# Optimization experiments

Measured on AMD Instinct MI355X. Metric: run time of the kernel, lower is better.

Reference implementation:

```python
import jax, jax.numpy as jnp
import numpy as np

HEADS = 12
LN_EPS = 1e-5


def setup_inputs() -> dict:
    B, S, D = 2, 2048, 768
    k = jax.random.key(0)
    ks = jax.random.split(k, 16)
    std = 0.02
    inp = {
        "key": jax.random.normal(ks[0], (B, S, D), jnp.float32),
        "query": jax.random.normal(ks[1], (B, S, D), jnp.float32),
        "value": jax.random.normal(ks[2], (B, S, D), jnp.float32),
        "mask": jax.random.randint(ks[3], (B, S, S), 0, 2).astype(bool),
        "Wk_w": jax.random.normal(ks[4], (D, D), jnp.float32) * std,
        "Wk_b": jnp.zeros((D,), jnp.float32),
        "Wq_w": jax.random.normal(ks[5], (D, D), jnp.float32) * std,
        "Wq_b": jnp.zeros((D,), jnp.float32),
        "Wv_w": jax.random.normal(ks[6], (D, D), jnp.float32) * std,
        "Wv_b": jnp.zeros((D,), jnp.float32),
        "Wc_w": jax.random.normal(ks[7], (D, D), jnp.float32) * std,
        "Wc_b": jnp.zeros((D,), jnp.float32),
        "ln_g": jnp.ones((D,), jnp.float32),
        "ln_b": jnp.zeros((D,), jnp.float32),
    }
    return inp


def _mha(key, query, value, mask, Wk_w, Wk_b, Wq_w, Wq_b, Wv_w, Wv_b,
         Wc_w, Wc_b, ln_g, ln_b):
    B, Sq, D = query.shape
    Sk = key.shape[1]
    H = HEADS
    hd = D // H
    scaler = np.float32(D ** 0.5)  # NOTE: source scales by sqrt(hidden_size), not sqrt(head_dim)

    # QKV projections (torch Linear: x @ W.T + b)
    hk = (key @ Wk_w.T + Wk_b).reshape(B, Sk, H, hd).transpose(2, 0, 1, 3)    # (H,B,Sk,hd)
    hq = (query @ Wq_w.T + Wq_b).reshape(B, Sq, H, hd).transpose(2, 0, 1, 3)  # (H,B,Sq,hd)
    hv = (value @ Wv_w.T + Wv_b).reshape(B, Sk, H, hd).transpose(2, 0, 1, 3)  # (H,B,Sk,hd)

    qk = jnp.einsum('hbqd,hbkd->hbqk', hq, hk) / scaler
    qk = jnp.where(mask[None], -jnp.inf, qk)  # mask repeated over heads in source
    attn = jax.nn.softmax(qk, axis=-1)        # dropout is identity in eval
    out = jnp.einsum('hbqk,hbkd->hbqd', attn, hv)  # (H,B,Sq,hd)

    # Faithful replication of source reshape chain:
    # (H*B,Sq,hd).view(B,H,Sq,hd).permute(1,2,0,3).view(B,Sq,D)
    out = out.reshape(B, H, Sq, hd)             # flat reinterpretation, head-major data
    out = jnp.transpose(out, (1, 2, 0, 3)).reshape(B, Sq, D)

    out = out @ Wc_w.T + Wc_b                   # Wconcat; dropout identity
    x = out + query                             # residual
    mu = jnp.mean(x, axis=-1, keepdims=True)
    var = jnp.mean((x - mu) ** 2, axis=-1, keepdims=True)
    return ln_g * (x - mu) / jnp.sqrt(var + LN_EPS) + ln_b


def reference(key, query, value, mask, Wk_w, Wk_b, Wq_w, Wq_b, Wv_w, Wv_b,
              Wc_w, Wc_b, ln_g, ln_b):
    return _mha(key, query, value, mask, Wk_w, Wk_b, Wq_w, Wq_b,
                Wv_w, Wv_b, Wc_w, Wc_b, ln_g, ln_b)
```

## Files before the change

### kernel.cpp

```cpp
#include <hip/hip_runtime.h>
#include <stdint.h>

typedef float v4f __attribute__((ext_vector_type(4)));
typedef short v8s __attribute__((ext_vector_type(8)));

#define AS1 __attribute__((address_space(1)))
#define AS3 __attribute__((address_space(3)))

__device__ __forceinline__ void load16_to_lds(const void* g, void* l) {
  __builtin_amdgcn_global_load_lds((AS1 void*)g, (AS3 void*)l, 16, 0, 0);
}
__device__ __forceinline__ void load4_to_lds(const void* g, void* l) {
  __builtin_amdgcn_global_load_lds((AS1 void*)g, (AS3 void*)l, 4, 0, 0);
}

__device__ __forceinline__ float fexp2(float x) {
#if __has_builtin(__builtin_amdgcn_exp2f)
  return __builtin_amdgcn_exp2f(x);
#else
  return exp2f(x);
#endif
}

__device__ __forceinline__ unsigned short f2bf_rn(float f) {
  union { float f; uint32_t u; } v; v.f = f;
  return (unsigned short)((v.u + 0x8000u) >> 16);
}
__device__ __forceinline__ uint32_t pack_bf2(float x, float y) {
  union { float f; uint32_t u; } a, b; a.f = x; b.f = y;
  return __builtin_amdgcn_perm(b.u + 0x8000u, a.u + 0x8000u, 0x07060302u);
}

#define QSCALE 0.052058786f

__global__ __launch_bounds__(256) void pack_mask_kernel(
    const uint32_t* __restrict__ mask, uint32_t* __restrict__ bits) {
  __shared__ int s_i32;
  const int tid = threadIdx.x;
  if (tid == 0) s_i32 = 1;
  __syncthreads();
  if (mask[tid] > 1u) s_i32 = 0;
  __syncthreads();
  if (s_i32) {
    const int lane = tid & 63;
    const int gw = (blockIdx.x * 256 + tid) >> 6;
#pragma unroll 4
    for (int it = 0; it < 32; ++it) {
      const size_t base = (size_t)gw * 2048 + it * 64;
      unsigned long long bal = __ballot(mask[base + lane] != 0u);
      if (lane == 0) *(unsigned long long*)&bits[base >> 5] = bal;
    }
  } else {
    const int wi = blockIdx.x * 256 + tid;
    const uint32_t* p = mask + (size_t)wi * 8;
    uint32_t w = 0;
#pragma unroll
    for (int j8 = 0; j8 < 8; ++j8) {
      uint32_t u = p[j8];
#pragma unroll
      for (int k = 0; k < 4; ++k)
        w |= (((u >> (8 * k)) & 0xFFu) ? 1u : 0u) << (j8 * 4 + k);
    }
    bits[wi] = w;
  }
}

__global__ __launch_bounds__(256) void conv_w_kernel(
    const float* __restrict__ wk, const float* __restrict__ wq,
    const float* __restrict__ wv, const float* __restrict__ wc,
    unsigned short* __restrict__ dk, unsigned short* __restrict__ dq,
    unsigned short* __restrict__ dv, unsigned short* __restrict__ dc) {
  const int y = blockIdx.y;
  const float* s; unsigned short* d; float sc = 1.f;
  if (y == 0)      { s = wk; d = dk; }
  else if (y == 1) { s = wq; d = dq; sc = QSCALE; }
  else if (y == 2) { s = wv; d = dv; }
  else             { s = wc; d = dc; }
  const int i = blockIdx.x * 256 + threadIdx.x;
  float4 f = ((const float4*)s)[i];
  uint2 o;
  o.x = pack_bf2(f.x * sc, f.y * sc);
  o.y = pack_bf2(f.z * sc, f.w * sc);
  ((uint2*)d)[i] = o;
}

__global__ __launch_bounds__(256) void gemm_qkv_kernel(
    const float* __restrict__ q_in, const float* __restrict__ k_in,
    const float* __restrict__ v_in,
    const unsigned short* __restrict__ wqb, const unsigned short* __restrict__ wkb,
    const unsigned short* __restrict__ wvb,
    const float* __restrict__ bq, const float* __restrict__ bk,
    const float* __restrict__ bv,
    unsigned short* __restrict__ Qb, unsigned short* __restrict__ Kb,
    unsigned short* __restrict__ Vt) {
  const int which = blockIdx.z;
  const float* A; const unsigned short* Wb; const float* bias; float bscale;
  if (which == 0)      { A = q_in; Wb = wqb; bias = bq; bscale = QSCALE; }
  else if (which == 1) { A = k_in; Wb = wkb; bias = bk; bscale = 1.f; }
  else                 { A = v_in; Wb = wvb; bias = bv; bscale = 1.f; }

  const int m0 = blockIdx.x * 128, n0 = blockIdx.y * 128;
  const int tid = threadIdx.x, lane = tid & 63, wid = tid >> 6;
  const int wm = wid >> 1, wn = wid & 1;
  const int l16 = lane & 15, quad = lane >> 4;

  __shared__ __align__(16) unsigned short As[128 * 32];
  __shared__ __align__(16) unsigned short Bs[128 * 32];

  v4f acc[4][4];
#pragma unroll
  for (int i = 0; i < 4; ++i)
#pragma unroll
    for (int j = 0; j < 4; ++j) { v4f z = {0.f, 0.f, 0.f, 0.f}; acc[i][j] = z; }

  for (int k0 = 0; k0 < 768; k0 += 32) {
#pragma unroll
    for (int i = 0; i < 4; ++i) {
      const int c = tid + i * 256;
      const int row = c >> 3, col4 = (c & 7) * 4;
      const float4 f = *(const float4*)&A[(size_t)(m0 + row) * 768 + k0 + col4];
      uint2 o; o.x = pack_bf2(f.x, f.y); o.y = pack_bf2(f.z, f.w);
      *(uint2*)&As[row * 32 + col4] = o;
    }
    {
      const int cbase = wid * 128;
#pragma unroll
      for (int iss = 0; iss < 2; ++iss) {
        const int c = cbase + iss * 64 + lane;
        const int row = c >> 2, col8 = (c & 3) * 8;
        load16_to_lds(Wb + (size_t)(n0 + row) * 768 + k0 + col8,
                      &Bs[(cbase + iss * 64) * 8]);
      }
    }
    __syncthreads();

    v8s af[4], bf[4];
#pragma unroll
    for (int i = 0; i < 4; ++i)
      af[i] = *(const v8s*)&As[(wm * 64 + i * 16 + l16) * 32 + quad * 8];
#pragma unroll
    for (int j = 0; j < 4; ++j)
      bf[j] = *(const v8s*)&Bs[(wn * 64 + j * 16 + l16) * 32 + quad * 8];
#pragma unroll
    for (int i = 0; i < 4; ++i)
#pragma unroll
      for (int j = 0; j < 4; ++j)
        acc[i][j] = __builtin_amdgcn_mfma_f32_16x16x32_bf16(af[i], bf[j],
                                                            acc[i][j], 0, 0, 0);
    __syncthreads();
  }

#pragma unroll
  for (int i = 0; i < 4; ++i) {
#pragma unroll
    for (int j = 0; j < 4; ++j) {
      const int mbase = m0 + wm * 64 + i * 16 + quad * 4;
      const int n = n0 + wn * 64 + j * 16 + l16;
      const float bv_ = bias[n] * bscale;
#pragma unroll
      for (int r = 0; r < 4; ++r) {
        const int m = mbase + r;
        const unsigned short hb = f2bf_rn(acc[i][j][r] + bv_);
        if (which == 0)      Qb[(size_t)m * 768 + n] = hb;
        else if (which == 1) Kb[(size_t)m * 768 + n] = hb;
        else {
          const int bb = m >> 11, ss = m & 2047;
          Vt[((size_t)bb * 768 + n) * 2048 + ss] = hb;
        }
      }
    }
  }
}

__global__ __launch_bounds__(256) void attn_kernel(
    const unsigned short* __restrict__ Qb, const unsigned short* __restrict__ Kb,
    const unsigned short* __restrict__ Vt, const uint32_t* __restrict__ mbits,
    unsigned short* __restrict__ X) {
  const int q0 = blockIdx.x * 64;
  const int h = blockIdx.y, b = blockIdx.z;
  const int tid = threadIdx.x, w = tid >> 6, lane = tid & 63;
  const int l16 = lane & 15, quad = lane >> 4, l7 = l16 & 7;

  __shared__ __align__(16) unsigned short Kl[64 * 64];
  __shared__ __align__(16) unsigned short Vl[64 * 64];
  __shared__ __align__(16) unsigned short Pl[4][16 * 64];
  __shared__ uint32_t Ml[128];

  v8s aq[2];
  {
    const unsigned short* qp =
        Qb + (size_t)(b * 2048 + q0 + w * 16 + l16) * 768 + h * 64 + quad * 8;
    aq[0] = *(const v8s*)qp;
    aq[1] = *(const v8s*)(qp + 32);
  }

  v4f o[4], ol;
#pragma unroll
  for (int nt = 0; nt < 4; ++nt) { v4f z = {0.f, 0.f, 0.f, 0.f}; o[nt] = z; }
  { v4f z = {0.f, 0.f, 0.f, 0.f}; ol = z; }

  v8s bones;
  {
    const short v1 = (l16 == 0) ? (short)0x3F80 : (short)0;
#pragma unroll
    for (int j = 0; j < 8; ++j) bones[j] = v1;
  }

  const int rsub = lane >> 3;
  const int csub = ((lane & 7) ^ rsub) * 8;

  for (int kk0 = 0; kk0 < 2048; kk0 += 64) {
    {
      const unsigned short* kg =
          Kb + (size_t)(b * 2048 + kk0 + w * 16) * 768 + h * 64;
      const unsigned short* vg =
          Vt + (size_t)(b * 768 + h * 64 + w * 16) * 2048 + kk0;
#pragma unroll
      for (int iss = 0; iss < 2; ++iss) {
        load16_to_lds(kg + (size_t)(iss * 8 + rsub) * 768 + csub,
                      &Kl[(w * 16 + iss * 8) * 64]);
        load16_to_lds(vg + (size_t)(iss * 8 + rsub) * 2048 + csub,
                      &Vl[(w * 16 + iss * 8) * 64]);
      }
      if (w < 2) {
        const uint32_t* mg = mbits +
            (size_t)(b * 2048 + q0 + w * 32 + (lane >> 1)) * 64 + (kk0 >> 5) +
            (lane & 1);
        load4_to_lds(mg, &Ml[w * 64]);
      }
    }
    __syncthreads();

    v4f sacc[4];
#pragma unroll
    for (int nt = 0; nt < 4; ++nt) { v4f z = {0.f, 0.f, 0.f, 0.f}; sacc[nt] = z; }
#pragma unroll
    for (int kt = 0; kt < 2; ++kt) {
      v8s bk[4];
#pragma unroll
      for (int nt = 0; nt < 4; ++nt)
        bk[nt] = *(const v8s*)&Kl[(nt * 16 + l16) * 64 +
                                  (((kt * 4 + quad) ^ l7) << 3)];
#pragma unroll
      for (int nt = 0; nt < 4; ++nt)
        sacc[nt] = __builtin_amdgcn_mfma_f32_16x16x32_bf16(aq[kt], bk[nt],
                                                           sacc[nt], 0, 0, 0);
    }

    const int rowb = w * 16 + quad * 4;
    const int hi = l16 >> 3;
#pragma unroll
    for (int r = 0; r < 4; ++r) {
      const uint32_t m0w = Ml[(rowb + r - w * 16 + w * 16) * 2];
      const uint32_t m1w = Ml[(rowb + r) * 2 + 1];
      const uint32_t u0 = m0w >> l16, u1 = m1w >> l16;
      const float p0 = (u0 & 1u) ? 0.f : fexp2(sacc[0][r]);
      const float p1 = ((u0 >> 16) & 1u) ? 0.f : fexp2(sacc[1][r]);
      const float p2 = (u1 & 1u) ? 0.f : fexp2(sacc[2][r]);
      const float p3 = ((u1 >> 16) & 1u) ? 0.f : fexp2(sacc[3][r]);
      const int prow = quad * 4 + r, ps = prow & 7;
      const int base = prow * 64 + l7;
      Pl[w][base + (((0 + hi) ^ ps) << 3)] = f2bf_rn(p0);
      Pl[w][base + (((2 + hi) ^ ps) << 3)] = f2bf_rn(p1);
      Pl[w][base + (((4 + hi) ^ ps) << 3)] = f2bf_rn(p2);
      Pl[w][base + (((6 + hi) ^ ps) << 3)] = f2bf_rn(p3);
    }

#pragma unroll
    for (int kt = 0; kt < 2; ++kt) {
      const v8s ap = *(const v8s*)&Pl[w][l16 * 64 + (((kt * 4 + quad) ^ l7) << 3)];
#pragma unroll
      for (int nt = 0; nt < 4; ++nt) {
        const v8s bv = *(const v8s*)&Vl[(nt * 16 + l16) * 64 +
                                        (((kt * 4 + quad) ^ l7) << 3)];
        o[nt] = __builtin_amdgcn_mfma_f32_16x16x32_bf16(ap, bv, o[nt], 0, 0, 0);
      }
      ol = __builtin_amdgcn_mfma_f32_16x16x32_bf16(ap, bones, ol, 0, 0, 0);
    }
    __syncthreads();
  }

  const int hb2 = 2 * h + b;
  const int b2 = (hb2 >= 12) ? 1 : 0;
  const int h2 = hb2 - 12 * b2;
#pragma unroll
  for (int r = 0; r < 4; ++r) {
    const float lsum = __shfl(ol[r], quad * 16, 64);
    const float inv_l = 1.f / lsum;
    const int q = q0 + w * 16 + quad * 4 + r;
#pragma unroll
    for (int nt = 0; nt < 4; ++nt) {
      const int d = nt * 16 + l16;
      const size_t f = (size_t)h2 * 262144 + (size_t)q * 128 + b2 * 64 + d;
      X[f] = f2bf_rn(o[nt][r] * inv_l);
    }
  }
}

__global__ __launch_bounds__(256) void gemm2_kernel(
    const unsigned short* __restrict__ X, const unsigned short* __restrict__ Wcb,
    const float* __restrict__ bc, const float* __restrict__ query,
    float* __restrict__ out) {
  const int m0 = blockIdx.x * 64, n0 = blockIdx.y * 128;
  const int tid = threadIdx.x, lane = tid & 63, wid = tid >> 6;
  const int wm = wid >> 1, wn = wid & 1;
  const int l16 = lane & 15, quad = lane >> 4;

  __shared__ __align__(16) unsigned short As[64 * 32];
  __shared__ __align__(16) unsigned short Bs[128 * 32];

  v4f acc[2][4];
#pragma unroll
  for (int i = 0; i < 2; ++i)
#pragma unroll
    for (int j = 0; j < 4; ++j) { v4f z = {0.f, 0.f, 0.f, 0.f}; acc[i][j] = z; }

  for (int k0 = 0; k0 < 768; k0 += 32) {
    load16_to_lds(X + (size_t)(m0 + (tid >> 2)) * 768 + k0 + (tid & 3) * 8,
                  &As[wid * 512]);
#pragma unroll
    for (int iss = 0; iss < 2; ++iss) {
      const int c = wid * 128 + iss * 64 + lane;
      const int row = c >> 2, col8 = (c & 3) * 8;
      load16_to_lds(Wcb + (size_t)(n0 + row) * 768 + k0 + col8,
                    &Bs[(wid * 128 + iss * 64) * 8]);
    }
    __syncthreads();

    v8s af[2], bf[4];
#pragma unroll
    for (int i = 0; i < 2; ++i)
      af[i] = *(const v8s*)&As[(wm * 32 + i * 16 + l16) * 32 + quad * 8];
#pragma unroll
    for (int j = 0; j < 4; ++j)
      bf[j] = *(const v8s*)&Bs[(wn * 64 + j * 16 + l16) * 32 + quad * 8];
#pragma unroll
    for (int i = 0; i < 2; ++i)
#pragma unroll
      for (int j = 0; j < 4; ++j)
        acc[i][j] = __builtin_amdgcn_mfma_f32_16x16x32_bf16(af[i], bf[j],
                                                            acc[i][j], 0, 0, 0);
    __syncthreads();
  }

#pragma unroll
  for (int i = 0; i < 2; ++i) {
#pragma unroll
    for (int j = 0; j < 4; ++j) {
      const int mbase = m0 + wm * 32 + i * 16 + quad * 4;
      const int n = n0 + wn * 64 + j * 16 + l16;
      const float bv_ = bc[n];
#pragma unroll
      for (int r = 0; r < 4; ++r) {
        const int m = mbase + r;
        out[(size_t)m * 768 + n] =
            acc[i][j][r] + bv_ + query[(size_t)m * 768 + n];
      }
    }
  }
}

__global__ __launch_bounds__(256) void ln_kernel(float* __restrict__ out,
                                                 const float* __restrict__ g,
                                                 const float* __restrict__ bta) {
  const int row = blockIdx.x;
  const int tid = threadIdx.x;
  float x[3];
  float s = 0.f, sq = 0.f;
#pragma unroll
  for (int k = 0; k < 3; ++k) {
    x[k] = out[(size_t)row * 768 + tid + k * 256];
    s += x[k];
    sq += x[k] * x[k];
  }
#pragma unroll
  for (int off = 1; off < 64; off <<= 1) {
    s += __shfl_xor(s, off, 64);
    sq += __shfl_xor(sq, off, 64);
  }
  __shared__ float ss[4], ssq[4];
  const int w = tid >> 6, lane = tid & 63;
  if (lane == 0) { ss[w] = s; ssq[w] = sq; }
  __syncthreads();
  s = ss[0] + ss[1] + ss[2] + ss[3];
  sq = ssq[0] + ssq[1] + ssq[2] + ssq[3];
  const float mu = s * (1.f / 768.f);
  const float var = sq * (1.f / 768.f) - mu * mu;
  const float rstd = rsqrtf(var + 1e-5f);
#pragma unroll
  for (int k = 0; k < 3; ++k) {
    const int cc = tid + k * 256;
    out[(size_t)row * 768 + cc] = g[cc] * (x[k] - mu) * rstd + bta[cc];
  }
}

extern "C" void kernel_launch(void* const* d_in, const int* in_sizes, int n_in,
                              void* d_out, int out_size, void* d_ws,
                              size_t ws_size, hipStream_t stream) {
  const float* key   = (const float*)d_in[0];
  const float* query = (const float*)d_in[1];
  const float* value = (const float*)d_in[2];
  const uint32_t* mask = (const uint32_t*)d_in[3];
  const float* Wk = (const float*)d_in[4];
  const float* bk = (const float*)d_in[5];
  const float* Wq = (const float*)d_in[6];
  const float* bq = (const float*)d_in[7];
  const float* Wv = (const float*)d_in[8];
  const float* bv = (const float*)d_in[9];
  const float* Wc = (const float*)d_in[10];
  const float* bc = (const float*)d_in[11];
  const float* lng = (const float*)d_in[12];
  const float* lnb = (const float*)d_in[13];

  char* ws = (char*)d_ws;
  uint32_t*       mbits = (uint32_t*)(ws);
  unsigned short* Wkb = (unsigned short*)(ws + 0x100000);
  unsigned short* Wqb = (unsigned short*)(ws + 0x220000);
  unsigned short* Wvb = (unsigned short*)(ws + 0x340000);
  unsigned short* Wcb = (unsigned short*)(ws + 0x460000);
  unsigned short* Qb  = (unsigned short*)(ws + 0x600000);
  unsigned short* Kb  = (unsigned short*)(ws + 0xC00000);
  unsigned short* Vt  = (unsigned short*)(ws + 0x1200000);
  unsigned short* X   = (unsigned short*)(ws + 0x1800000);
  float* out = (float*)d_out;

  pack_mask_kernel<<<dim3(1024), dim3(256), 0, stream>>>(mask, mbits);
  conv_w_kernel<<<dim3(576, 4), dim3(256), 0, stream>>>(Wk, Wq, Wv, Wc,
                                                        Wkb, Wqb, Wvb, Wcb);
  gemm_qkv_kernel<<<dim3(32, 6, 3), dim3(256), 0, stream>>>(
      query, key, value, Wqb, Wkb, Wvb, bq, bk, bv, Qb, Kb, Vt);
  attn_kernel<<<dim3(32, 12, 2), dim3(256), 0, stream>>>(Qb, Kb, Vt, mbits, X);
  gemm2_kernel<<<dim3(64, 6), dim3(256), 0, stream>>>(X, Wcb, bc, query, out);
  ln_kernel<<<dim3(4096), dim3(256), 0, stream>>>(out, lng, lnb);
}
```

Baseline: 249.5 us.

## Double-buffer LDS in GEMMs and attention, pre-convert activations to bf16

Each GEMM and the attention loop now use double-buffered LDS. The next tile is issued with async global-to-LDS loads before the current tile's MFMAs, and one barrier per iteration replaces two. The key/query/value fp32 inputs are converted to bf16 in a separate pass, stored in scratch space borrowed from the output buffer and the X buffer. This lets the QKV GEMM load A through direct LDS loads instead of per-thread convert-and-store. V-transpose stores are also packed into 8-byte writes, and occupancy hints are added. The risks are an extra full pass over the activations and more LDS per block.

```diff
diff --git a/kernel.cpp b/kernel.cpp
--- a/kernel.cpp
+++ b/kernel.cpp
@@ -65,18 +65,28 @@
   }
 }
 
-__global__ __launch_bounds__(256) void conv_w_kernel(
+__global__ __launch_bounds__(256) void conv_kernel(
     const float* __restrict__ wk, const float* __restrict__ wq,
     const float* __restrict__ wv, const float* __restrict__ wc,
+    const float* __restrict__ kin, const float* __restrict__ qin,
+    const float* __restrict__ vin,
     unsigned short* __restrict__ dk, unsigned short* __restrict__ dq,
-    unsigned short* __restrict__ dv, unsigned short* __restrict__ dc) {
+    unsigned short* __restrict__ dv, unsigned short* __restrict__ dc,
+    unsigned short* __restrict__ dki, unsigned short* __restrict__ dqi,
+    unsigned short* __restrict__ dvi) {
   const int y = blockIdx.y;
-  const float* s; unsigned short* d; float sc = 1.f;
-  if (y == 0)      { s = wk; d = dk; }
-  else if (y == 1) { s = wq; d = dq; sc = QSCALE; }
-  else if (y == 2) { s = wv; d = dv; }
-  else             { s = wc; d = dc; }
+  const float* s; unsigned short* d; float sc = 1.f; int n4;
+  switch (y) {
+    case 0: s = wk;  d = dk;  n4 = 147456; break;
+    case 1: s = wq;  d = dq;  n4 = 147456; sc = QSCALE; break;
+    case 2: s = wv;  d = dv;  n4 = 147456; break;
+    case 3: s = wc;  d = dc;  n4 = 147456; break;
+    case 4: s = kin; d = dki; n4 = 786432; break;
+    case 5: s = qin; d = dqi; n4 = 786432; break;
+    default: s = vin; d = dvi; n4 = 786432; break;
+  }
   const int i = blockIdx.x * 256 + threadIdx.x;
+  if (i >= n4) return;
   float4 f = ((const float4*)s)[i];
   uint2 o;
   o.x = pack_bf2(f.x * sc, f.y * sc);
@@ -84,9 +94,9 @@
   ((uint2*)d)[i] = o;
 }
 
-__global__ __launch_bounds__(256) void gemm_qkv_kernel(
-    const float* __restrict__ q_in, const float* __restrict__ k_in,
-    const float* __restrict__ v_in,
+__global__ __launch_bounds__(256, 3) void gemm_qkv_kernel(
+    const unsigned short* __restrict__ qin, const unsigned short* __restrict__ kin,
+    const unsigned short* __restrict__ vin,
     const unsigned short* __restrict__ wqb, const unsigned short* __restrict__ wkb,
     const unsigned short* __restrict__ wvb,
     const float* __restrict__ bq, const float* __restrict__ bk,
@@ -94,18 +104,19 @@
     unsigned short* __restrict__ Qb, unsigned short* __restrict__ Kb,
     unsigned short* __restrict__ Vt) {
   const int which = blockIdx.z;
-  const float* A; const unsigned short* Wb; const float* bias; float bscale;
-  if (which == 0)      { A = q_in; Wb = wqb; bias = bq; bscale = QSCALE; }
-  else if (which == 1) { A = k_in; Wb = wkb; bias = bk; bscale = 1.f; }
-  else                 { A = v_in; Wb = wvb; bias = bv; bscale = 1.f; }
+  const unsigned short* A; const unsigned short* Wb; const float* bias;
+  float bscale = 1.f;
+  if (which == 0)      { A = qin; Wb = wqb; bias = bq; bscale = QSCALE; }
+  else if (which == 1) { A = kin; Wb = wkb; bias = bk; }
+  else                 { A = vin; Wb = wvb; bias = bv; }
 
   const int m0 = blockIdx.x * 128, n0 = blockIdx.y * 128;
   const int tid = threadIdx.x, lane = tid & 63, wid = tid >> 6;
   const int wm = wid >> 1, wn = wid & 1;
   const int l16 = lane & 15, quad = lane >> 4;
 
-  __shared__ __align__(16) unsigned short As[128 * 32];
-  __shared__ __align__(16) unsigned short Bs[128 * 32];
+  __shared__ __align__(16) unsigned short As[2][128 * 32];
+  __shared__ __align__(16) unsigned short Bs[2][128 * 32];
 
   v4f acc[4][4];
 #pragma unroll
@@ -113,42 +124,41 @@
 #pragma unroll
     for (int j = 0; j < 4; ++j) { v4f z = {0.f, 0.f, 0.f, 0.f}; acc[i][j] = z; }
 
-  for (int k0 = 0; k0 < 768; k0 += 32) {
-#pragma unroll
-    for (int i = 0; i < 4; ++i) {
-      const int c = tid + i * 256;
-      const int row = c >> 3, col4 = (c & 7) * 4;
-      const float4 f = *(const float4*)&A[(size_t)(m0 + row) * 768 + k0 + col4];
-      uint2 o; o.x = pack_bf2(f.x, f.y); o.y = pack_bf2(f.z, f.w);
-      *(uint2*)&As[row * 32 + col4] = o;
-    }
-    {
-      const int cbase = wid * 128;
-#pragma unroll
-      for (int iss = 0; iss < 2; ++iss) {
-        const int c = cbase + iss * 64 + lane;
-        const int row = c >> 2, col8 = (c & 3) * 8;
-        load16_to_lds(Wb + (size_t)(n0 + row) * 768 + k0 + col8,
-                      &Bs[(cbase + iss * 64) * 8]);
-      }
-    }
+  const int c0 = wid * 128 + lane, c1 = wid * 128 + 64 + lane;
+  const unsigned short* a0 = A + (size_t)(m0 + (c0 >> 2)) * 768 + (c0 & 3) * 8;
+  const unsigned short* a1 = A + (size_t)(m0 + (c1 >> 2)) * 768 + (c1 & 3) * 8;
+  const unsigned short* b0 = Wb + (size_t)(n0 + (c0 >> 2)) * 768 + (c0 & 3) * 8;
+  const unsigned short* b1 = Wb + (size_t)(n0 + (c1 >> 2)) * 768 + (c1 & 3) * 8;
+
+#define QKV_STAGE(k0, buf)                                         \
+  do {                                                             \
+    load16_to_lds(a0 + (k0), &As[buf][(wid * 128) * 8]);           \
+    load16_to_lds(a1 + (k0), &As[buf][(wid * 128 + 64) * 8]);      \
+    load16_to_lds(b0 + (k0), &Bs[buf][(wid * 128) * 8]);           \
+    load16_to_lds(b1 + (k0), &Bs[buf][(wid * 128 + 64) * 8]);      \
+  } while (0)
+
+  QKV_STAGE(0, 0);
+#pragma unroll 2
+  for (int ks = 0; ks < 24; ++ks) {
+    const int bufc = ks & 1;
     __syncthreads();
-
     v8s af[4], bf[4];
 #pragma unroll
     for (int i = 0; i < 4; ++i)
-      af[i] = *(const v8s*)&As[(wm * 64 + i * 16 + l16) * 32 + quad * 8];
+      af[i] = *(const v8s*)&As[bufc][(wm * 64 + i * 16 + l16) * 32 + quad * 8];
 #pragma unroll
     for (int j = 0; j < 4; ++j)
-      bf[j] = *(const v8s*)&Bs[(wn * 64 + j * 16 + l16) * 32 + quad * 8];
+      bf[j] = *(const v8s*)&Bs[bufc][(wn * 64 + j * 16 + l16) * 32 + quad * 8];
+    if (ks < 23) QKV_STAGE((ks + 1) * 32, bufc ^ 1);
 #pragma unroll
     for (int i = 0; i < 4; ++i)
 #pragma unroll
       for (int j = 0; j < 4; ++j)
         acc[i][j] = __builtin_amdgcn_mfma_f32_16x16x32_bf16(af[i], bf[j],
                                                             acc[i][j], 0, 0, 0);
-    __syncthreads();
-  }
+  }
+#undef QKV_STAGE
 
 #pragma unroll
   for (int i = 0; i < 4; ++i) {
@@ -157,22 +167,23 @@
       const int mbase = m0 + wm * 64 + i * 16 + quad * 4;
       const int n = n0 + wn * 64 + j * 16 + l16;
       const float bv_ = bias[n] * bscale;
-#pragma unroll
-      for (int r = 0; r < 4; ++r) {
-        const int m = mbase + r;
-        const unsigned short hb = f2bf_rn(acc[i][j][r] + bv_);
-        if (which == 0)      Qb[(size_t)m * 768 + n] = hb;
-        else if (which == 1) Kb[(size_t)m * 768 + n] = hb;
-        else {
-          const int bb = m >> 11, ss = m & 2047;
-          Vt[((size_t)bb * 768 + n) * 2048 + ss] = hb;
-        }
+      if (which == 2) {
+        const int bb = mbase >> 11, ss = mbase & 2047;
+        uint2 pk;
+        pk.x = pack_bf2(acc[i][j][0] + bv_, acc[i][j][1] + bv_);
+        pk.y = pack_bf2(acc[i][j][2] + bv_, acc[i][j][3] + bv_);
+        *(uint2*)&Vt[((size_t)bb * 768 + n) * 2048 + ss] = pk;
+      } else {
+        unsigned short* dst = (which == 0) ? Qb : Kb;
+#pragma unroll
+        for (int r = 0; r < 4; ++r)
+          dst[(size_t)(mbase + r) * 768 + n] = f2bf_rn(acc[i][j][r] + bv_);
       }
     }
   }
 }
 
-__global__ __launch_bounds__(256) void attn_kernel(
+__global__ __launch_bounds__(256, 3) void attn_kernel(
     const unsigned short* __restrict__ Qb, const unsigned short* __restrict__ Kb,
     const unsigned short* __restrict__ Vt, const uint32_t* __restrict__ mbits,
     unsigned short* __restrict__ X) {
@@ -181,10 +192,10 @@
   const int tid = threadIdx.x, w = tid >> 6, lane = tid & 63;
   const int l16 = lane & 15, quad = lane >> 4, l7 = l16 & 7;
 
-  __shared__ __align__(16) unsigned short Kl[64 * 64];
-  __shared__ __align__(16) unsigned short Vl[64 * 64];
+  __shared__ __align__(16) unsigned short Kl[2][64 * 64];
+  __shared__ __align__(16) unsigned short Vl[2][64 * 64];
   __shared__ __align__(16) unsigned short Pl[4][16 * 64];
-  __shared__ uint32_t Ml[128];
+  __shared__ uint32_t Ml[2][128];
 
   v8s aq[2];
   {
@@ -208,52 +219,55 @@
 
   const int rsub = lane >> 3;
   const int csub = ((lane & 7) ^ rsub) * 8;
-
-  for (int kk0 = 0; kk0 < 2048; kk0 += 64) {
-    {
-      const unsigned short* kg =
-          Kb + (size_t)(b * 2048 + kk0 + w * 16) * 768 + h * 64;
-      const unsigned short* vg =
-          Vt + (size_t)(b * 768 + h * 64 + w * 16) * 2048 + kk0;
-#pragma unroll
-      for (int iss = 0; iss < 2; ++iss) {
-        load16_to_lds(kg + (size_t)(iss * 8 + rsub) * 768 + csub,
-                      &Kl[(w * 16 + iss * 8) * 64]);
-        load16_to_lds(vg + (size_t)(iss * 8 + rsub) * 2048 + csub,
-                      &Vl[(w * 16 + iss * 8) * 64]);
-      }
-      if (w < 2) {
-        const uint32_t* mg = mbits +
-            (size_t)(b * 2048 + q0 + w * 32 + (lane >> 1)) * 64 + (kk0 >> 5) +
-            (lane & 1);
-        load4_to_lds(mg, &Ml[w * 64]);
-      }
-    }
+  const unsigned short* kg0 = Kb + (size_t)(b * 2048 + w * 16) * 768 + h * 64;
+  const unsigned short* vg0 = Vt + (size_t)(b * 768 + h * 64 + w * 16) * 2048;
+  const uint32_t* mg0 =
+      mbits + (size_t)(b * 2048 + q0 + w * 32 + (lane >> 1)) * 64 + (lane & 1);
+
+#define ATTN_STAGE(kk0, buf)                                                  \
+  do {                                                                        \
+    const unsigned short* kg = kg0 + (size_t)(kk0) * 768;                     \
+    const unsigned short* vg = vg0 + (kk0);                                   \
+    load16_to_lds(kg + (size_t)rsub * 768 + csub, &Kl[buf][(w * 16) * 64]);   \
+    load16_to_lds(kg + (size_t)(8 + rsub) * 768 + csub,                       \
+                  &Kl[buf][(w * 16 + 8) * 64]);                               \
+    load16_to_lds(vg + (size_t)rsub * 2048 + csub, &Vl[buf][(w * 16) * 64]);  \
+    load16_to_lds(vg + (size_t)(8 + rsub) * 2048 + csub,                      \
+                  &Vl[buf][(w * 16 + 8) * 64]);                               \
+    if (w < 2) load4_to_lds(mg0 + ((kk0) >> 5), &Ml[buf][w * 64]);            \
+  } while (0)
+
+  ATTN_STAGE(0, 0);
+#pragma unroll 2
+  for (int it = 0; it < 32; ++it) {
+    const int bufc = it & 1;
     __syncthreads();
 
+    v8s bk[2][4];
+#pragma unroll
+    for (int kt = 0; kt < 2; ++kt)
+#pragma unroll
+      for (int nt = 0; nt < 4; ++nt)
+        bk[kt][nt] = *(const v8s*)&Kl[bufc][(nt * 16 + l16) * 64 +
+                                           (((kt * 4 + quad) ^ l7) << 3)];
+    if (it < 31) ATTN_STAGE((it + 1) * 64, bufc ^ 1);
+
     v4f sacc[4];
 #pragma unroll
     for (int nt = 0; nt < 4; ++nt) { v4f z = {0.f, 0.f, 0.f, 0.f}; sacc[nt] = z; }
 #pragma unroll
-    for (int kt = 0; kt < 2; ++kt) {
-      v8s bk[4];
+    for (int kt = 0; kt < 2; ++kt)
 #pragma unroll
       for (int nt = 0; nt < 4; ++nt)
-        bk[nt] = *(const v8s*)&Kl[(nt * 16 + l16) * 64 +
-                                  (((kt * 4 + quad) ^ l7) << 3)];
-#pragma unroll
-      for (int nt = 0; nt < 4; ++nt)
-        sacc[nt] = __builtin_amdgcn_mfma_f32_16x16x32_bf16(aq[kt], bk[nt],
+        sacc[nt] = __builtin_amdgcn_mfma_f32_16x16x32_bf16(aq[kt], bk[kt][nt],
                                                            sacc[nt], 0, 0, 0);
-    }
 
     const int rowb = w * 16 + quad * 4;
     const int hi = l16 >> 3;
 #pragma unroll
     for (int r = 0; r < 4; ++r) {
-      const uint32_t m0w = Ml[(rowb + r - w * 16 + w * 16) * 2];
-      const uint32_t m1w = Ml[(rowb + r) * 2 + 1];
-      const uint32_t u0 = m0w >> l16, u1 = m1w >> l16;
+      const uint2 mw = *(const uint2*)&Ml[bufc][(rowb + r - w * 16 + w * 16) * 2];
+      const uint32_t u0 = mw.x >> l16, u1 = mw.y >> l16;
       const float p0 = (u0 & 1u) ? 0.f : fexp2(sacc[0][r]);
       const float p1 = ((u0 >> 16) & 1u) ? 0.f : fexp2(sacc[1][r]);
       const float p2 = (u1 & 1u) ? 0.f : fexp2(sacc[2][r]);
@@ -271,14 +285,14 @@
       const v8s ap = *(const v8s*)&Pl[w][l16 * 64 + (((kt * 4 + quad) ^ l7) << 3)];
 #pragma unroll
       for (int nt = 0; nt < 4; ++nt) {
-        const v8s bv = *(const v8s*)&Vl[(nt * 16 + l16) * 64 +
-                                        (((kt * 4 + quad) ^ l7) << 3)];
+        const v8s bv = *(const v8s*)&Vl[bufc][(nt * 16 + l16) * 64 +
+                                             (((kt * 4 + quad) ^ l7) << 3)];
         o[nt] = __builtin_amdgcn_mfma_f32_16x16x32_bf16(ap, bv, o[nt], 0, 0, 0);
       }
       ol = __builtin_amdgcn_mfma_f32_16x16x32_bf16(ap, bones, ol, 0, 0, 0);
     }
-    __syncthreads();
-  }
+  }
+#undef ATTN_STAGE
 
   const int hb2 = 2 * h + b;
   const int b2 = (hb2 >= 12) ? 1 : 0;
@@ -297,7 +311,7 @@
   }
 }
 
-__global__ __launch_bounds__(256) void gemm2_kernel(
+__global__ __launch_bounds__(256, 3) void gemm2_kernel(
     const unsigned short* __restrict__ X, const unsigned short* __restrict__ Wcb,
     const float* __restrict__ bc, const float* __restrict__ query,
     float* __restrict__ out) {
@@ -306,8 +320,8 @@
   const int wm = wid >> 1, wn = wid & 1;
   const int l16 = lane & 15, quad = lane >> 4;
 
-  __shared__ __align__(16) unsigned short As[64 * 32];
-  __shared__ __align__(16) unsigned short Bs[128 * 32];
+  __shared__ __align__(16) unsigned short As[2][64 * 32];
+  __shared__ __align__(16) unsigned short Bs[2][128 * 32];
 
   v4f acc[2][4];
 #pragma unroll
@@ -315,33 +329,40 @@
 #pragma unroll
     for (int j = 0; j < 4; ++j) { v4f z = {0.f, 0.f, 0.f, 0.f}; acc[i][j] = z; }
 
-  for (int k0 = 0; k0 < 768; k0 += 32) {
-    load16_to_lds(X + (size_t)(m0 + (tid >> 2)) * 768 + k0 + (tid & 3) * 8,
-                  &As[wid * 512]);
-#pragma unroll
-    for (int iss = 0; iss < 2; ++iss) {
-      const int c = wid * 128 + iss * 64 + lane;
-      const int row = c >> 2, col8 = (c & 3) * 8;
-      load16_to_lds(Wcb + (size_t)(n0 + row) * 768 + k0 + col8,
-                    &Bs[(wid * 128 + iss * 64) * 8]);
-    }
+  const int ca = tid;
+  const unsigned short* a0 = X + (size_t)(m0 + (ca >> 2)) * 768 + (ca & 3) * 8;
+  const int c0 = wid * 128 + lane, c1 = wid * 128 + 64 + lane;
+  const unsigned short* b0 = Wcb + (size_t)(n0 + (c0 >> 2)) * 768 + (c0 & 3) * 8;
+  const unsigned short* b1 = Wcb + (size_t)(n0 + (c1 >> 2)) * 768 + (c1 & 3) * 8;
+
+#define G2_STAGE(k0, buf)                                        \
+  do {                                                           \
+    load16_to_lds(a0 + (k0), &As[buf][(wid * 64) * 8]);          \
+    load16_to_lds(b0 + (k0), &Bs[buf][(wid * 128) * 8]);         \
+    load16_to_lds(b1 + (k0), &Bs[buf][(wid * 128 + 64) * 8]);    \
+  } while (0)
+
+  G2_STAGE(0, 0);
+#pragma unroll 2
+  for (int ks = 0; ks < 24; ++ks) {
+    const int bufc = ks & 1;
     __syncthreads();
-
     v8s af[2], bf[4];
 #pragma unroll
     for (int i = 0; i < 2; ++i)
-      af[i] = *(const v8s*)&As[(wm * 32 + i * 16 + l16) * 32 + quad * 8];
+      af[i] = *(const v8s*)&As[bufc][(wm * 32 + i * 16 + l16) * 32 + quad * 8];
 #pragma unroll
     for (int j = 0; j < 4; ++j)
-      bf[j] = *(const v8s*)&Bs[(wn * 64 + j * 16 + l16) * 32 + quad * 8];
+      bf[j] = *(const v8s*)&Bs[bufc][(wn * 64 + j * 16 + l16) * 32 + quad * 8];
+    if (ks < 23) G2_STAGE((ks + 1) * 32, bufc ^ 1);
 #pragma unroll
     for (int i = 0; i < 2; ++i)
 #pragma unroll
       for (int j = 0; j < 4; ++j)
         acc[i][j] = __builtin_amdgcn_mfma_f32_16x16x32_bf16(af[i], bf[j],
                                                             acc[i][j], 0, 0, 0);
-    __syncthreads();
-  }
+  }
+#undef G2_STAGE
 
 #pragma unroll
   for (int i = 0; i < 2; ++i) {
@@ -422,13 +443,17 @@
   unsigned short* Kb  = (unsigned short*)(ws + 0xC00000);
   unsigned short* Vt  = (unsigned short*)(ws + 0x1200000);
   unsigned short* X   = (unsigned short*)(ws + 0x1800000);
+  unsigned short* Kin = (unsigned short*)d_out;
+  unsigned short* Qin = (unsigned short*)d_out + 3145728;
+  unsigned short* Vin = X;
   float* out = (float*)d_out;
 
   pack_mask_kernel<<<dim3(1024), dim3(256), 0, stream>>>(mask, mbits);
-  conv_w_kernel<<<dim3(576, 4), dim3(256), 0, stream>>>(Wk, Wq, Wv, Wc,
-                                                        Wkb, Wqb, Wvb, Wcb);
+  conv_kernel<<<dim3(3072, 7), dim3(256), 0, stream>>>(
+      Wk, Wq, Wv, Wc, key, query, value,
+      Wkb, Wqb, Wvb, Wcb, Kin, Qin, Vin);
   gemm_qkv_kernel<<<dim3(32, 6, 3), dim3(256), 0, stream>>>(
-      query, key, value, Wqb, Wkb, Wvb, bq, bk, bv, Qb, Kb, Vt);
+      Qin, Kin, Vin, Wqb, Wkb, Wvb, bq, bk, bv, Qb, Kb, Vt);
   attn_kernel<<<dim3(32, 12, 2), dim3(256), 0, stream>>>(Qb, Kb, Vt, mbits, X);
   gemm2_kernel<<<dim3(64, 6), dim3(256), 0, stream>>>(X, Wcb, bc, query, out);
   ln_kernel<<<dim3(4096), dim3(256), 0, stream>>>(out, lng, lnb);
```

Result: faster. 243.9 us (-2.3%).
